# Kernel optimization log

Measured on AMD Instinct MI355X. Metric: run time of the kernel, lower is better.

## Reference

```python
import jax, jax.numpy as jnp
from jax import lax
import numpy as np

NPOINT = 1024   # S: number of sampled centroids
RADIUS = 0.3
NSAMPLE = 32    # K: neighbors per ball
EPS = 1e-5      # BatchNorm eps
B, N, D = 4, 16384, 64


def farthest_point_sample(xyz, npoint):
    # xyz: [B, N, 3] -> idx [B, npoint]; deterministic start at index 0
    Bb, Nn, _ = xyz.shape
    def step(carry, _):
        distance, farthest = carry  # [B,N], [B]
        centroid = jnp.take_along_axis(xyz, farthest[:, None, None], axis=1)  # [B,1,3]
        d = jnp.sum((xyz - centroid) ** 2, axis=-1)  # [B,N]
        distance = jnp.minimum(distance, d)
        nxt = jnp.argmax(distance, axis=-1).astype(jnp.int32)
        return (distance, nxt), farthest
    init = (jnp.full((Bb, Nn), 1e10, xyz.dtype), jnp.zeros((Bb,), jnp.int32))
    _, idxs = lax.scan(step, init, None, length=npoint)  # [npoint, B]
    return jnp.transpose(idxs)


def query_ball_point(radius, nsample, xyz, new_xyz):
    # xyz [B,N,3], new_xyz [B,S,3] -> idx [B,S,nsample]
    Bb, Nn, _ = xyz.shape
    sqr = jnp.sum((new_xyz[:, :, None, :] - xyz[:, None, :, :]) ** 2, axis=-1)  # [B,S,N]
    gidx = jnp.broadcast_to(jnp.arange(Nn, dtype=jnp.int32), sqr.shape)
    gidx = jnp.where(sqr > radius * radius, Nn, gidx)
    gidx = jnp.sort(gidx, axis=-1)[:, :, :nsample]
    first = gidx[:, :, 0:1]  # centroid itself (dist 0) always qualifies
    return jnp.where(gidx == Nn, first, gidx)


def index_points(points, idx):
    # points [B,N,C], idx [B,...] -> [B,...,C]
    return jax.vmap(lambda p, i: p[i])(points, idx)


def mlp_layer(x, w, b, g, beta):
    # x [B,S,K,Cin]; 1x1 conv == per-point matmul; BN (train stats) over (B,S,K); ReLU
    y = jnp.einsum('bskc,oc->bsko', x, w) + b
    mean = jnp.mean(y, axis=(0, 1, 2))
    var = jnp.var(y, axis=(0, 1, 2))
    y = (y - mean) * lax.rsqrt(var + EPS) * g + beta
    return jax.nn.relu(y)


def setup_inputs() -> dict:
    key = jax.random.key(0)
    ks = jax.random.split(key, 5)
    return {
        'xyz': jax.random.normal(ks[0], (B, 3, N), jnp.float32),
        'points': jax.random.normal(ks[1], (B, D, N), jnp.float32),
        'w1': jax.random.normal(ks[2], (64, 67), jnp.float32) * 0.1,
        'b1': jnp.zeros((64,), jnp.float32),
        'g1': jnp.ones((64,), jnp.float32),
        'bt1': jnp.zeros((64,), jnp.float32),
        'w2': jax.random.normal(ks[3], (64, 64), jnp.float32) * 0.1,
        'b2': jnp.zeros((64,), jnp.float32),
        'g2': jnp.ones((64,), jnp.float32),
        'bt2': jnp.zeros((64,), jnp.float32),
        'w3': jax.random.normal(ks[4], (128, 64), jnp.float32) * 0.1,
        'b3': jnp.zeros((128,), jnp.float32),
        'g3': jnp.ones((128,), jnp.float32),
        'bt3': jnp.zeros((128,), jnp.float32),
    }


def reference(xyz, points, w1, b1, g1, bt1, w2, b2, g2, bt2, w3, b3, g3, bt3):
    xyz_t = jnp.transpose(xyz, (0, 2, 1))      # [B,N,3]
    pts_t = jnp.transpose(points, (0, 2, 1))   # [B,N,D]
    fps_idx = farthest_point_sample(xyz_t, NPOINT)          # [B,S]
    new_xyz = index_points(xyz_t, fps_idx)                  # [B,S,3]
    idx = query_ball_point(RADIUS, NSAMPLE, xyz_t, new_xyz) # [B,S,K]
    grouped_xyz = index_points(xyz_t, idx) - new_xyz[:, :, None, :]  # [B,S,K,3]
    grouped_pts = index_points(pts_t, idx)                  # [B,S,K,D]
    x = jnp.concatenate([grouped_xyz, grouped_pts], axis=-1)  # [B,S,K,3+D]
    x = mlp_layer(x, w1, b1, g1, bt1)
    x = mlp_layer(x, w2, b2, g2, bt2)
    x = mlp_layer(x, w3, b3, g3, bt3)
    new_points = jnp.max(x, axis=2)  # max over K neighbors -> [B,S,128]
    return (jnp.transpose(new_xyz, (0, 2, 1)), jnp.transpose(new_points, (0, 2, 1)))
```

## Files before the change

kernel.cpp:

```cpp
#include <hip/hip_runtime.h>
#include <hip/hip_bf16.h>
#include <stdint.h>

#define NPT   16384
#define BB    4
#define SS    1024
#define KK    32
#define RR    (BB*SS*KK)
#define C1    67
#define O1    64
#define O3    128
#define EPSF  1e-5f
#define R2F   0.09f
#define FT    1024
#define FE    16
#define BIGI  0x7fffffff

#define REP16(M) M(0) M(1) M(2) M(3) M(4) M(5) M(6) M(7) \
                 M(8) M(9) M(10) M(11) M(12) M(13) M(14) M(15)
#define REP16R(M) M(15) M(14) M(13) M(12) M(11) M(10) M(9) M(8) \
                  M(7) M(6) M(5) M(4) M(3) M(2) M(1) M(0)

#define WMAX5(v) { \
    v = fmaxf(v, __int_as_float(__builtin_amdgcn_ds_swizzle(__float_as_int(v), 0x041F))); \
    v = fmaxf(v, __int_as_float(__builtin_amdgcn_ds_swizzle(__float_as_int(v), 0x081F))); \
    v = fmaxf(v, __int_as_float(__builtin_amdgcn_ds_swizzle(__float_as_int(v), 0x101F))); \
    v = fmaxf(v, __int_as_float(__builtin_amdgcn_ds_swizzle(__float_as_int(v), 0x201F))); \
    v = fmaxf(v, __int_as_float(__builtin_amdgcn_ds_swizzle(__float_as_int(v), 0x401F))); }

__global__ __launch_bounds__(FT)
__attribute__((amdgpu_waves_per_eu(4, 4)))
void k_fps(const float* __restrict__ xyz, int* __restrict__ fps_idx) {
    const int b = blockIdx.x;
    const int tid = threadIdx.x;
    const int lane = tid & 63;
    const float* xb = xyz + (size_t)b * 3 * NPT;

    __shared__ float2 sxy[NPT];
    __shared__ int s_M[2];
    __shared__ unsigned long long s_wz[2];

#define DECLV(i) float Z##i, D##i;
    REP16(DECLV)
#define INITV(i) { int n = (i) * FT + tid; \
                   float xx = xb[n]; \
                   float yy = xb[NPT + n]; \
                   float zz = xb[2 * NPT + n]; \
                   sxy[n] = make_float2(xx, yy); \
                   asm volatile("" : "+v"(zz)); \
                   Z##i = zz; D##i = 1e10f; }
    REP16(INITV)
    if (tid == 0) { s_M[0] = 0; s_M[1] = 0; s_wz[0] = ~0ull; s_wz[1] = ~0ull; }
    __syncthreads();

    int p = 0;
    int far = 0;
    float2 c0 = sxy[0];
    float cx = c0.x, cy = c0.y, cz = xb[2 * NPT];
    for (int it = 0; it < SS; ++it) {
        if (tid == 0) fps_idx[b * SS + it] = far;
#define UPDV(i) { float2 xy = sxy[(i) * FT + tid]; \
                  float dx = __fsub_rn(xy.x, cx); \
                  float dy = __fsub_rn(xy.y, cy); \
                  float dz = __fsub_rn(Z##i, cz); \
                  float d = __fadd_rn(__fadd_rn(__fmul_rn(dx, dx), __fmul_rn(dy, dy)), \
                                      __fmul_rn(dz, dz)); \
                  D##i = fminf(D##i, d); }
        REP16(UPDV)
        float m0 = fmaxf(fmaxf(D0, D1), fmaxf(D2, D3));
        float m1 = fmaxf(fmaxf(D4, D5), fmaxf(D6, D7));
        float m2 = fmaxf(fmaxf(D8, D9), fmaxf(D10, D11));
        float m3 = fmaxf(fmaxf(D12, D13), fmaxf(D14, D15));
        float tbd = fmaxf(fmaxf(m0, m1), fmaxf(m2, m3));

        float bd = tbd;
        WMAX5(bd)
        bd = fmaxf(bd, __shfl_xor(bd, 32));
        if (lane == 0) atomicMax(&s_M[p], __float_as_int(bd));
        __syncthreads();
        if (tid == 0) { s_M[p ^ 1] = 0; s_wz[p ^ 1] = ~0ull; }
        float Mf = __int_as_float(s_M[p]);
        if (tbd == Mf) {
            int bn = BIGI; float zw = 0.0f;
#define SCANV(i) { bool m = (D##i == Mf); \
                   bn = m ? ((i) * FT + tid) : bn; \
                   zw = m ? Z##i : zw; }
            REP16R(SCANV)
            atomicMin(&s_wz[p], ((unsigned long long)(unsigned)bn << 32) |
                                (unsigned long long)__float_as_uint(zw));
        }
        __syncthreads();
        unsigned long long wz = s_wz[p];
        far = (int)(wz >> 32);
        cz = __uint_as_float((unsigned)wz);
        float2 cxy = sxy[far];
        cx = cxy.x; cy = cxy.y;
        p ^= 1;
    }
#undef DECLV
#undef INITV
#undef UPDV
#undef SCANV
}

__global__ void k_newxyz(const float* __restrict__ xyz, const int* __restrict__ fps_idx,
                         float* __restrict__ out0, float* __restrict__ nxyz) {
    int g = blockIdx.x * blockDim.x + threadIdx.x;
    if (g >= BB * SS) return;
    int b = g / SS, s = g % SS;
    int id = fps_idx[g];
    const float* xb = xyz + (size_t)b * 3 * NPT;
#pragma unroll
    for (int c = 0; c < 3; ++c) {
        float v = xb[c * NPT + id];
        out0[(size_t)b * 3 * SS + c * SS + s] = v;
        nxyz[g * 3 + c] = v;
    }
}

__global__ __launch_bounds__(256) void k_ball(const float* __restrict__ xyz,
                                              const float* __restrict__ nxyz,
                                              int* __restrict__ ballidx) {
    int wid = (blockIdx.x * 256 + threadIdx.x) >> 6;
    int lane = threadIdx.x & 63;
    int b = wid >> 10;
    const float* xb = xyz + (size_t)b * 3 * NPT;
    float nx = nxyz[wid * 3], ny = nxyz[wid * 3 + 1], nz = nxyz[wid * 3 + 2];
    int* out = ballidx + (size_t)wid * KK;
    int cnt = 0;
    int first = -1;
    for (int base = 0; base < NPT; base += 64) {
        int n = base + lane;
        float dx = __fsub_rn(nx, xb[n]);
        float dy = __fsub_rn(ny, xb[NPT + n]);
        float dz = __fsub_rn(nz, xb[2 * NPT + n]);
        float d = __fadd_rn(__fadd_rn(__fmul_rn(dx, dx), __fmul_rn(dy, dy)),
                            __fmul_rn(dz, dz));
        bool hit = !(d > R2F);
        unsigned long long mask = __ballot(hit);
        if (mask) {
            if (first < 0) first = base + __builtin_ctzll(mask);
            int rank = cnt + __popcll(mask & ((1ull << lane) - 1ull));
            if (hit && rank < KK) out[rank] = n;
            cnt += __popcll(mask);
        }
        if (cnt >= KK) break;
    }
    if (lane >= cnt && lane < KK) out[lane] = first;
}

__global__ __launch_bounds__(256) void k_tr(const float* __restrict__ pts,
                                            float* __restrict__ ptsT) {
    __shared__ float t[64][65];
    int b = blockIdx.x >> 8, n0 = (blockIdx.x & 255) << 6;
    const float* pb = pts + (size_t)b * 64 * NPT;
    int tx = threadIdx.x & 63, ty = threadIdx.x >> 6;
#pragma unroll
    for (int k = 0; k < 16; ++k) {
        int c = ty * 16 + k;
        t[c][tx] = pb[(size_t)c * NPT + n0 + tx];
    }
    __syncthreads();
#pragma unroll
    for (int k = 0; k < 16; ++k) {
        int n = ty * 16 + k;
        ptsT[((size_t)b * NPT + n0 + n) * 64 + tx] = t[tx][n];
    }
}

__global__ __launch_bounds__(256)
__attribute__((amdgpu_waves_per_eu(1, 4)))
void k_gemm1(const float* __restrict__ xyz,
        const float* __restrict__ ptsT, const float* __restrict__ nxyz,
        const int* __restrict__ ballidx, const float* __restrict__ w,
        const float* __restrict__ bias, float* __restrict__ Y,
        float* __restrict__ sumP, float* __restrict__ sqP) {
    __shared__ float wlds[C1 * O1];
    __shared__ float blds[O1];
    __shared__ float lsum[4][O1];
    __shared__ float lsq[4][O1];
    for (int i = threadIdx.x; i < C1 * O1; i += 256) {
        int c = i >> 6, o = i & 63;
        wlds[i] = w[o * C1 + c];
    }
    if (threadIdx.x < O1) blds[threadIdx.x] = bias[threadIdx.x];
    __syncthreads();
    int r = blockIdx.x * 256 + threadIdx.x;
    int b = r >> 15;
    int g = r >> 5;
    int id = ballidx[r];
    const float* xb = xyz + (size_t)b * 3 * NPT;
    float acc[O1];
#pragma unroll
    for (int o = 0; o < O1; ++o) acc[o] = blds[o];
#pragma unroll
    for (int c = 0; c < 3; ++c) {
        float xv = xb[c * NPT + id] - nxyz[g * 3 + c];
        const float* wr = &wlds[c * O1];
#pragma unroll
        for (int o = 0; o < O1; ++o) acc[o] = fmaf(xv, wr[o], acc[o]);
    }
    const float4* p4 = (const float4*)(ptsT + ((size_t)b * NPT + id) * 64);
#pragma unroll 4
    for (int cc = 0; cc < 16; ++cc) {
        float4 x = p4[cc];
        float xs[4] = {x.x, x.y, x.z, x.w};
#pragma unroll
        for (int u = 0; u < 4; ++u) {
            const float* wr = &wlds[(3 + cc * 4 + u) * O1];
#pragma unroll
            for (int o = 0; o < O1; ++o) acc[o] = fmaf(xs[u], wr[o], acc[o]);
        }
    }
    float4* yr = (float4*)(Y + (size_t)r * O1);
#pragma unroll
    for (int o4 = 0; o4 < O1 / 4; ++o4)
        yr[o4] = make_float4(acc[o4 * 4], acc[o4 * 4 + 1], acc[o4 * 4 + 2], acc[o4 * 4 + 3]);
    int lane = threadIdx.x & 63, wvv = threadIdx.x >> 6;
#pragma unroll
    for (int o = 0; o < O1; ++o) {
        float v = acc[o], v2 = acc[o] * acc[o];
#pragma unroll
        for (int off = 1; off < 64; off <<= 1) { v += __shfl_xor(v, off); v2 += __shfl_xor(v2, off); }
        if (lane == 0) { lsum[wvv][o] = v; lsq[wvv][o] = v2; }
    }
    __syncthreads();
    if (threadIdx.x < O1) {
        int o = threadIdx.x;
        sumP[blockIdx.x * O1 + o] = lsum[0][o] + lsum[1][o] + lsum[2][o] + lsum[3][o];
        sqP[blockIdx.x * O1 + o]  = lsq[0][o] + lsq[1][o] + lsq[2][o] + lsq[3][o];
    }
}

template <int CIN, int OTOT, bool NORM_IN, bool WRITE_Y, bool PARTIALS, bool MAXOUT>
__global__ __launch_bounds__(256)
__attribute__((amdgpu_waves_per_eu(1, 4)))
void k_mlp(
        const float* __restrict__ Yin, const float* __restrict__ w,
        const float* __restrict__ bias, const float* __restrict__ isc,
        const float* __restrict__ ish, float* __restrict__ Yout,
        float* __restrict__ sumP, float* __restrict__ sqP,
        float* __restrict__ ymax) {
    const int h = blockIdx.y;
    const int ob = h * 64;
    __shared__ float wlds[CIN * 64];
    __shared__ float blds[64];
    __shared__ float iscl[NORM_IN ? CIN : 1], ishl[NORM_IN ? CIN : 1];
    __shared__ float lsum[PARTIALS ? 4 : 1][PARTIALS ? 64 : 1];
    __shared__ float lsq[PARTIALS ? 4 : 1][PARTIALS ? 64 : 1];
    for (int i = threadIdx.x; i < CIN * 64; i += 256) {
        int c = i >> 6, o = i & 63;
        wlds[i] = w[(ob + o) * CIN + c];
    }
    if (threadIdx.x < 64) blds[threadIdx.x] = bias[ob + threadIdx.x];
    if (NORM_IN) {
        for (int i = threadIdx.x; i < CIN; i += 256) { iscl[i] = isc[i]; ishl[i] = ish[i]; }
    }
    __syncthreads();
    int r = blockIdx.x * 256 + threadIdx.x;
    float acc[64];
#pragma unroll
    for (int o = 0; o < 64; ++o) acc[o] = blds[o];
    const float4* r4 = (const float4*)(Yin + (size_t)r * CIN);
#pragma unroll 4
    for (int cc = 0; cc < CIN / 4; ++cc) {
        float4 x = r4[cc];
        float xs[4] = {x.x, x.y, x.z, x.w};
#pragma unroll
        for (int u = 0; u < 4; ++u) {
            int c = cc * 4 + u;
            float xv = xs[u];
            if (NORM_IN) xv = fmaxf(fmaf(xv, iscl[c], ishl[c]), 0.0f);
            const float* wr = &wlds[c * 64];
#pragma unroll
            for (int o = 0; o < 64; ++o) acc[o] = fmaf(xv, wr[o], acc[o]);
        }
    }
    if (WRITE_Y) {
        float4* yr = (float4*)(Yout + (size_t)r * OTOT + ob);
#pragma unroll
        for (int o4 = 0; o4 < 16; ++o4)
            yr[o4] = make_float4(acc[o4 * 4], acc[o4 * 4 + 1], acc[o4 * 4 + 2], acc[o4 * 4 + 3]);
    }
    if (PARTIALS) {
        int lane = threadIdx.x & 63, wvv = threadIdx.x >> 6;
#pragma unroll
        for (int o = 0; o < 64; ++o) {
            float v = acc[o], v2 = acc[o] * acc[o];
#pragma unroll
            for (int off = 1; off < 64; off <<= 1) { v += __shfl_xor(v, off); v2 += __shfl_xor(v2, off); }
            if (lane == 0) { lsum[wvv][o] = v; lsq[wvv][o] = v2; }
        }
        __syncthreads();
        if (threadIdx.x < 64) {
            int o = threadIdx.x;
            sumP[blockIdx.x * OTOT + ob + o] = lsum[0][o] + lsum[1][o] + lsum[2][o] + lsum[3][o];
            sqP[blockIdx.x * OTOT + ob + o]  = lsq[0][o] + lsq[1][o] + lsq[2][o] + lsq[3][o];
        }
    }
    if (MAXOUT) {
        int b = r >> 15, s = (r >> 5) & (SS - 1);
#pragma unroll
        for (int o = 0; o < 64; ++o) {
            float v = acc[o];
#pragma unroll
            for (int off = 1; off < 32; off <<= 1) v = fmaxf(v, __shfl_xor(v, off));
            if ((threadIdx.x & 31) == 0)
                ymax[((size_t)b * O3 + ob + o) * SS + s] = v;
        }
    }
}

__global__ __launch_bounds__(256) void k_pool(const float* __restrict__ ymax,
                                              const float* __restrict__ sc,
                                              const float* __restrict__ sh,
                                              float* __restrict__ out1) {
    int i = blockIdx.x * 256 + threadIdx.x;
    int o = (i >> 10) & (O3 - 1);
    out1[i] = fmaxf(fmaf(ymax[i], sc[o], sh[o]), 0.0f);
}

template <int COUT>
__global__ void k_finalize(const float* __restrict__ sumP, const float* __restrict__ sqP,
                           const float* __restrict__ g, const float* __restrict__ beta,
                           float* __restrict__ scale, float* __restrict__ shift) {
    __shared__ float ls[4][COUT], lq[4][COUT];
    int o = threadIdx.x % COUT, q = threadIdx.x / COUT;
    float s = 0.f, qq = 0.f;
    for (int bk = q; bk < 512; bk += 4) { s += sumP[bk * COUT + o]; qq += sqP[bk * COUT + o]; }
    ls[q][o] = s; lq[q][o] = qq;
    __syncthreads();
    if (q == 0) {
        s  = ls[0][o] + ls[1][o] + ls[2][o] + ls[3][o];
        qq = lq[0][o] + lq[1][o] + lq[2][o] + lq[3][o];
        const float inv = 1.0f / (float)RR;
        float mean = s * inv;
        float var = qq * inv - mean * mean;
        float sc = g[o] * rsqrtf(var + EPSF);
        scale[o] = sc;
        shift[o] = beta[o] - mean * sc;
    }
}

extern "C" void kernel_launch(void* const* d_in, const int* in_sizes, int n_in,
                              void* d_out, int out_size, void* d_ws, size_t ws_size,
                              hipStream_t stream) {
    const float* xyz = (const float*)d_in[0];
    const float* pts = (const float*)d_in[1];
    const float* w1  = (const float*)d_in[2];
    const float* b1  = (const float*)d_in[3];
    const float* g1  = (const float*)d_in[4];
    const float* bt1 = (const float*)d_in[5];
    const float* w2  = (const float*)d_in[6];
    const float* b2  = (const float*)d_in[7];
    const float* g2  = (const float*)d_in[8];
    const float* bt2 = (const float*)d_in[9];
    const float* w3  = (const float*)d_in[10];
    const float* b3  = (const float*)d_in[11];
    const float* g3  = (const float*)d_in[12];
    const float* bt3 = (const float*)d_in[13];
    float* out0 = (float*)d_out;
    float* out1 = out0 + BB * 3 * SS;

    char* wsb = (char*)d_ws;
    size_t off = 0;
    auto alloc = [&](size_t bytes) {
        char* p = wsb + off;
        off += (bytes + 255) & ~(size_t)255;
        return p;
    };
    int*   fps_idx = (int*)alloc((size_t)BB * SS * 4);
    int*   ballidx = (int*)alloc((size_t)RR * 4);
    float* nxyz    = (float*)alloc((size_t)BB * SS * 3 * 4);
    float* sumP    = (float*)alloc((size_t)512 * 128 * 4);
    float* sqP     = (float*)alloc((size_t)512 * 128 * 4);
    float* sc1     = (float*)alloc(128 * 4);
    float* sh1     = (float*)alloc(128 * 4);
    float* sc2     = (float*)alloc(128 * 4);
    float* sh2     = (float*)alloc(128 * 4);
    float* sc3     = (float*)alloc(128 * 4);
    float* sh3     = (float*)alloc(128 * 4);
    float* ymax    = (float*)alloc((size_t)BB * O3 * SS * 4);
    float* Y1      = (float*)alloc((size_t)RR * 64 * 4);
    float* Y2      = (float*)alloc((size_t)RR * 64 * 4);
    float* ptsT    = Y2;

    k_tr<<<1024, 256, 0, stream>>>(pts, ptsT);
    k_fps<<<BB, FT, 0, stream>>>(xyz, fps_idx);
    k_newxyz<<<16, 256, 0, stream>>>(xyz, fps_idx, out0, nxyz);
    k_ball<<<1024, 256, 0, stream>>>(xyz, nxyz, ballidx);

    k_gemm1<<<512, 256, 0, stream>>>(xyz, ptsT, nxyz, ballidx, w1, b1, Y1, sumP, sqP);
    k_finalize<64><<<1, 256, 0, stream>>>(sumP, sqP, g1, bt1, sc1, sh1);

    k_mlp<64, 64, true, true, true, false><<<dim3(512, 1), 256, 0, stream>>>(
        Y1, w2, b2, sc1, sh1, Y2, sumP, sqP, nullptr);
    k_finalize<64><<<1, 256, 0, stream>>>(sumP, sqP, g2, bt2, sc2, sh2);

    k_mlp<64, 128, true, false, true, true><<<dim3(512, 2), 256, 0, stream>>>(
        Y2, w3, b3, sc2, sh2, nullptr, sumP, sqP, ymax);
    k_finalize<128><<<1, 512, 0, stream>>>(sumP, sqP, g3, bt3, sc3, sh3);

    k_pool<<<BB * O3 * SS / 256, 256, 0, stream>>>(ymax, sc3, sh3, out1);
}
```

Baseline: 1.801 ms.

## Fuse points transpose into FPS launch and replace atomic max with LDS reduction

The separate transpose kernel becomes extra blocks of the FPS kernel, so the transpose runs on idle CUs alongside the 4 long-running FPS blocks instead of as its own launch. Inside the FPS loop, the per-wave atomicMax into shared memory is replaced by each wave writing its max to an LDS slot, which every lane then reduces with swizzles. This drops the reset of the max slot and the atomic contention. Transpose blocks now use 1024 threads and share the FPS kernel's large LDS allocation, which may limit how many of them fit per CU.

```diff
diff --git a/kernel.cpp b/kernel.cpp
--- a/kernel.cpp
+++ b/kernel.cpp
@@ -30,15 +30,37 @@
 
 __global__ __launch_bounds__(FT)
 __attribute__((amdgpu_waves_per_eu(4, 4)))
-void k_fps(const float* __restrict__ xyz, int* __restrict__ fps_idx) {
+void k_fps(const float* __restrict__ xyz, int* __restrict__ fps_idx,
+           const float* __restrict__ pts, float* __restrict__ ptsT) {
+    const int tid = threadIdx.x;
+    const int lane = tid & 63, wv = tid >> 6;
+
+    __shared__ float2 sxy[NPT];
+    __shared__ float s_red[16];
+    __shared__ unsigned long long s_wz[2];
+
+    if (blockIdx.x >= BB) {
+        int bid = blockIdx.x - BB;
+        int b = bid >> 8, n0 = (bid & 255) << 6;
+        float* t = (float*)sxy;
+        const float* pb = pts + (size_t)b * 64 * NPT;
+        int tx = tid & 63, ty = tid >> 6;
+#pragma unroll
+        for (int k = 0; k < 4; ++k) {
+            int c = ty * 4 + k;
+            t[c * 65 + tx] = pb[(size_t)c * NPT + n0 + tx];
+        }
+        __syncthreads();
+#pragma unroll
+        for (int k = 0; k < 4; ++k) {
+            int n = ty * 4 + k;
+            ptsT[((size_t)b * NPT + n0 + n) * 64 + tx] = t[tx * 65 + n];
+        }
+        return;
+    }
+
     const int b = blockIdx.x;
-    const int tid = threadIdx.x;
-    const int lane = tid & 63;
     const float* xb = xyz + (size_t)b * 3 * NPT;
-
-    __shared__ float2 sxy[NPT];
-    __shared__ int s_M[2];
-    __shared__ unsigned long long s_wz[2];
 
 #define DECLV(i) float Z##i, D##i;
     REP16(DECLV)
@@ -50,7 +72,7 @@
                    asm volatile("" : "+v"(zz)); \
                    Z##i = zz; D##i = 1e10f; }
     REP16(INITV)
-    if (tid == 0) { s_M[0] = 0; s_M[1] = 0; s_wz[0] = ~0ull; s_wz[1] = ~0ull; }
+    if (tid == 0) { s_wz[0] = ~0ull; s_wz[1] = ~0ull; }
     __syncthreads();
 
     int p = 0;
@@ -76,10 +98,14 @@
         float bd = tbd;
         WMAX5(bd)
         bd = fmaxf(bd, __shfl_xor(bd, 32));
-        if (lane == 0) atomicMax(&s_M[p], __float_as_int(bd));
+        if (lane == 0) s_red[wv] = bd;
         __syncthreads();
-        if (tid == 0) { s_M[p ^ 1] = 0; s_wz[p ^ 1] = ~0ull; }
-        float Mf = __int_as_float(s_M[p]);
+        if (tid == 0) s_wz[p ^ 1] = ~0ull;
+        float Mf = s_red[lane & 15];
+        Mf = fmaxf(Mf, __int_as_float(__builtin_amdgcn_ds_swizzle(__float_as_int(Mf), 0x041F)));
+        Mf = fmaxf(Mf, __int_as_float(__builtin_amdgcn_ds_swizzle(__float_as_int(Mf), 0x081F)));
+        Mf = fmaxf(Mf, __int_as_float(__builtin_amdgcn_ds_swizzle(__float_as_int(Mf), 0x101F)));
+        Mf = fmaxf(Mf, __int_as_float(__builtin_amdgcn_ds_swizzle(__float_as_int(Mf), 0x201F)));
         if (tbd == Mf) {
             int bn = BIGI; float zw = 0.0f;
 #define SCANV(i) { bool m = (D##i == Mf); \
@@ -149,25 +175,6 @@
     if (lane >= cnt && lane < KK) out[lane] = first;
 }
 
-__global__ __launch_bounds__(256) void k_tr(const float* __restrict__ pts,
-                                            float* __restrict__ ptsT) {
-    __shared__ float t[64][65];
-    int b = blockIdx.x >> 8, n0 = (blockIdx.x & 255) << 6;
-    const float* pb = pts + (size_t)b * 64 * NPT;
-    int tx = threadIdx.x & 63, ty = threadIdx.x >> 6;
-#pragma unroll
-    for (int k = 0; k < 16; ++k) {
-        int c = ty * 16 + k;
-        t[c][tx] = pb[(size_t)c * NPT + n0 + tx];
-    }
-    __syncthreads();
-#pragma unroll
-    for (int k = 0; k < 16; ++k) {
-        int n = ty * 16 + k;
-        ptsT[((size_t)b * NPT + n0 + n) * 64 + tx] = t[tx][n];
-    }
-}
-
 __global__ __launch_bounds__(256)
 __attribute__((amdgpu_waves_per_eu(1, 4)))
 void k_gemm1(const float* __restrict__ xyz,
@@ -385,8 +392,7 @@
     float* Y2      = (float*)alloc((size_t)RR * 64 * 4);
     float* ptsT    = Y2;
 
-    k_tr<<<1024, 256, 0, stream>>>(pts, ptsT);
-    k_fps<<<BB, FT, 0, stream>>>(xyz, fps_idx);
+    k_fps<<<BB + 1024, FT, 0, stream>>>(xyz, fps_idx, pts, ptsT);
     k_newxyz<<<16, 256, 0, stream>>>(xyz, fps_idx, out0, nxyz);
     k_ball<<<1024, 256, 0, stream>>>(xyz, nxyz, ballidx);
 
```

After: 1.861 ms. 3.3% more time.
